# Kernel optimization log

Hardware: AMD Instinct MI355X
Metric: run time of the kernel (lower is better)

Reference implementation:

```python
import jax, jax.numpy as jnp
import numpy as np

T, B, E, H = 2048, 4, 768, 12
HD = E // H


def setup_inputs() -> dict:
    root = jax.random.key(0)
    ks = jax.random.split(root, 7)
    def xavier(k, shape):
        fan_in, fan_out = shape[1], shape[0]
        lim = (6.0 / (fan_in + fan_out)) ** 0.5
        return jax.random.uniform(k, shape, jnp.float32, -lim, lim)
    return {
        "query": jax.random.normal(ks[0], (T, B, E), jnp.float32),
        "key": jax.random.normal(ks[1], (T, B, E), jnp.float32),
        "value": jax.random.normal(ks[2], (T, B, E), jnp.float32),
        "in_proj_weight": xavier(ks[3], (3 * E, E)),
        "in_proj_bias": jnp.zeros((3 * E,), jnp.float32),
        "out_w": xavier(ks[4], (E, E)),
        "out_b": jnp.zeros((E,), jnp.float32),
    }


def reference(query, key, value, in_proj_weight, in_proj_bias, out_w, out_b):
    scaling = HD ** -0.5
    # separate Q/K/V projections from slices of the fused in_proj weight
    q = (query @ in_proj_weight[:E].T + in_proj_bias[:E]) * scaling
    k = key @ in_proj_weight[E:2 * E].T + in_proj_bias[E:2 * E]
    v = value @ in_proj_weight[2 * E:].T + in_proj_bias[2 * E:]
    tgt_len, bsz, _ = query.shape
    src_len = key.shape[0]
    # [T,B,E] -> [B,H,T,hd]
    qh = q.reshape(tgt_len, bsz, H, HD).transpose(1, 2, 0, 3)
    kh = k.reshape(src_len, bsz, H, HD).transpose(1, 2, 0, 3)
    vh = v.reshape(src_len, bsz, H, HD).transpose(1, 2, 0, 3)
    # full attention matrix [B,H,T,S] (faithful to the bmm-softmax-bmm impl)
    scores = jnp.einsum("bhqd,bhkd->bhqk", qh, kh)
    weights = jax.nn.softmax(scores, axis=-1)  # attn_dropout = 0.0 (eval)
    attn = jnp.einsum("bhqk,bhkd->bhqd", weights, vh)
    attn = attn.transpose(2, 0, 1, 3).reshape(tgt_len, bsz, E)
    out = attn @ out_w.T + out_b
    avg_weights = weights.sum(axis=1) / H  # [B,T,S]
    return out, avg_weights
```

## Files before the change

### kernel.cpp

```cpp
#include <hip/hip_runtime.h>

typedef unsigned short u16;
typedef unsigned long long u64;
typedef __attribute__((ext_vector_type(8))) short bf16x8;
typedef __attribute__((ext_vector_type(4))) float f32x4;
typedef __attribute__((ext_vector_type(16))) float f32x16;
typedef __attribute__((ext_vector_type(4))) _Float16 f16x4;
typedef __attribute__((ext_vector_type(2))) __fp16 h16x2;

#define TT 2048
#define BB 4
#define EE 768
#define HH 12
#define HD 64
#define NTOK 8192
#define KVB 32
#define NTILE (TT / KVB)

__device__ __forceinline__ u16 f2bf(float f) {
  unsigned int u = __builtin_bit_cast(unsigned int, f);
  u += 0x7fffu + ((u >> 16) & 1u);
  return (u16)(u >> 16);
}

__device__ __forceinline__ float bf2f(u16 b) {
  unsigned int u = (unsigned int)b << 16;
  return __builtin_bit_cast(float, u);
}

__device__ __forceinline__ unsigned int pack2(u16 a, u16 b) {
  return (unsigned int)a | ((unsigned int)b << 16);
}

__device__ __forceinline__ unsigned int pkh2(float a, float b) {
  h16x2 t = __builtin_amdgcn_cvt_pkrtz(a, b);
  return __builtin_bit_cast(unsigned int, t);
}

__global__ __launch_bounds__(256) void proj_qkv(
    const float* __restrict__ q_in, const float* __restrict__ k_in, const float* __restrict__ v_in,
    const float* __restrict__ ipw, const float* __restrict__ ipb,
    u16* __restrict__ qh, u16* __restrict__ kh, u16* __restrict__ vh)
{
  __shared__ u16 sA[128 * 40];
  __shared__ u16 sB[192 * 40];
  const int tid = threadIdx.x;
  const int w = tid >> 6, lane = tid & 63, l32 = lane & 31, hi = lane >> 5;
  const int wm = w & 1, wn = w >> 1;
  const int bn = blockIdx.x, bm = blockIdx.y, z = blockIdx.z;

  const float* A = (z == 0) ? q_in : (z == 1) ? k_in : v_in;
  const float* W = ipw + (size_t)z * EE * EE;
  const float* bias = ipb + z * EE;

  f32x16 acc[2][3] = {};

  for (int kt = 0; kt < EE / 32; ++kt) {
    __syncthreads();
#pragma unroll
    for (int i = 0; i < 4; ++i) {
      int c = i * 256 + tid;
      int row = c >> 3, cs = c & 7;
      const float4 v4 = *(const float4*)(A + (size_t)(bm * 128 + row) * EE + kt * 32 + cs * 4);
      u64 pk = (u64)pack2(f2bf(v4.x), f2bf(v4.y)) |
               ((u64)pack2(f2bf(v4.z), f2bf(v4.w)) << 32);
      *(u64*)&sA[row * 40 + cs * 4] = pk;
    }
#pragma unroll
    for (int i = 0; i < 6; ++i) {
      int c = i * 256 + tid;
      int row = c >> 3, cs = c & 7;
      const float4 v4 = *(const float4*)(W + (size_t)(bn * 192 + row) * EE + kt * 32 + cs * 4);
      u64 pk = (u64)pack2(f2bf(v4.x), f2bf(v4.y)) |
               ((u64)pack2(f2bf(v4.z), f2bf(v4.w)) << 32);
      *(u64*)&sB[row * 40 + cs * 4] = pk;
    }
    __syncthreads();
#pragma unroll
    for (int ks = 0; ks < 2; ++ks) {
      bf16x8 bfr[3];
#pragma unroll
      for (int tn = 0; tn < 3; ++tn)
        bfr[tn] = *(const bf16x8*)&sB[(wn * 96 + tn * 32 + l32) * 40 + ks * 16 + hi * 8];
#pragma unroll
      for (int tm = 0; tm < 2; ++tm) {
        bf16x8 afr = *(const bf16x8*)&sA[(wm * 64 + tm * 32 + l32) * 40 + ks * 16 + hi * 8];
#pragma unroll
        for (int tn = 0; tn < 3; ++tn)
          acc[tm][tn] = __builtin_amdgcn_mfma_f32_32x32x16_bf16(afr, bfr[tn], acc[tm][tn], 0, 0, 0);
      }
    }
  }

  const float scale = (z == 0) ? 0.125f : 1.0f;
  u16* dst = (z == 0) ? qh : (z == 1) ? kh : vh;
#pragma unroll
  for (int tn = 0; tn < 3; ++tn) {
    const int j = bn * 192 + wn * 96 + tn * 32 + l32;
    const int h = j >> 6, d = j & 63;
    const float bj = bias[j];
#pragma unroll
    for (int tm = 0; tm < 2; ++tm) {
#pragma unroll
      for (int r = 0; r < 16; ++r) {
        int m = bm * 128 + wm * 64 + tm * 32 + (r & 3) + 8 * (r >> 2) + 4 * hi;
        int t = m >> 2, bb = m & 3;
        float v = (acc[tm][tn][r] + bj) * scale;
        dst[((size_t)((bb * HH + h) * TT + t)) * HD + d] = f2bf(v);
      }
    }
  }
}

__global__ __launch_bounds__(256) void transpose_v(
    const u16* __restrict__ vh, _Float16* __restrict__ vhT)
{
  __shared__ u16 tile[64][72];
  const int tid = threadIdx.x;
  const int bh = blockIdx.y;
  const int t0 = blockIdx.x * 64;
  {
    int row = tid >> 2, seg = tid & 3;
    const u16* src = vh + (size_t)bh * TT * HD + (size_t)(t0 + row) * HD + seg * 16;
    uint4 a = *(const uint4*)(src);
    uint4 b = *(const uint4*)(src + 8);
    *(uint4*)&tile[row][seg * 16] = a;
    *(uint4*)&tile[row][seg * 16 + 8] = b;
  }
  __syncthreads();
  {
    int d = tid >> 2, ts = tid & 3;
    u16 tmp[16];
#pragma unroll
    for (int i = 0; i < 16; ++i) tmp[i] = tile[ts * 16 + i][d];
    unsigned int pk[8];
#pragma unroll
    for (int i = 0; i < 8; ++i)
      pk[i] = pkh2(bf2f(tmp[2 * i]), bf2f(tmp[2 * i + 1]));
    uint4 o0, o1;
    o0.x = pk[0]; o0.y = pk[1]; o0.z = pk[2]; o0.w = pk[3];
    o1.x = pk[4]; o1.y = pk[5]; o1.z = pk[6]; o1.w = pk[7];
    _Float16* dst = vhT + (size_t)bh * HD * TT + (size_t)d * TT + t0 + ts * 16;
    *(uint4*)dst = o0;
    *(uint4*)(dst + 8) = o1;
  }
}

__global__ __launch_bounds__(256, 3) void attn_flash(
    const u16* __restrict__ qh, const u16* __restrict__ kh, const _Float16* __restrict__ vhT,
    u16* __restrict__ ctx, float* __restrict__ stats_rl)
{
  __shared__ u16 sK[2][KVB * 64];
  __shared__ _Float16 sV[2][64 * 36];

  const int tid = threadIdx.x, w = tid >> 6, lane = tid & 63;
  const int l16 = lane & 15, quad = lane >> 4;
  const int orig = blockIdx.x;
  const int wg = (orig & 7) * 96 + (orig >> 3);
  const int qb = wg & 15;
  const int bhl = wg >> 4;
  const int b = bhl / HH, h = bhl - b * HH;
  const int q0 = qb * 128 + w * 32;
  const size_t bh = (size_t)bhl;
  const u16* qg = qh + (bh * TT + q0) * HD;
  const u16* kg = kh + bh * TT * HD;
  const _Float16* vg = vhT + bh * HD * TT;

  const int krow = tid >> 3, kch = tid & 7;
  const int kdst = krow * 64 + ((kch ^ (krow & 7)) * 8);
  const u16* kgp = kg + (size_t)krow * HD + kch * 8;
  const int vrow = tid >> 2, vch = tid & 3;
  const int vdst = vrow * 36 + vch * 8;
  const _Float16* vgp = vg + (size_t)vrow * TT + vch * 8;

  bf16x8 qf[2][2];
#pragma unroll
  for (int j = 0; j < 2; ++j)
#pragma unroll
    for (int p = 0; p < 2; ++p)
      qf[j][p] = *(const bf16x8*)(qg + (j * 16 + l16) * HD + p * 32 + quad * 8);

  f32x4 oacc[2][4] = {};
  float lsum[2] = {0.0f, 0.0f};

  {
    uint4 kv = *(const uint4*)kgp;
    uint4 vv = *(const uint4*)vgp;
    *(uint4*)&sK[0][kdst] = kv;
    *(u64*)&sV[0][vdst]     = ((const u64*)&vv)[0];
    *(u64*)&sV[0][vdst + 4] = ((const u64*)&vv)[1];
  }

  for (int st = 0; st < NTILE; ++st) {
    const int buf = st & 1;
    uint4 nk, nv;
    const bool more = (st + 1 < NTILE);
    if (more) {
      nk = *(const uint4*)(kgp + (size_t)(st + 1) * KVB * HD);
      nv = *(const uint4*)(vgp + (st + 1) * KVB);
    }
    __syncthreads();

    const u16* kb = &sK[buf][0];
    const _Float16* vb = &sV[buf][0];
#pragma unroll
    for (int ss = 0; ss < 2; ++ss) {
      const int krw = ss * 16 + l16;
      bf16x8 kf0 = *(const bf16x8*)&kb[krw * 64 + ((quad ^ (krw & 7)) * 8)];
      bf16x8 kf1 = *(const bf16x8*)&kb[krw * 64 + (((4 + quad) ^ (krw & 7)) * 8)];
      f16x4 vf[4];
#pragma unroll
      for (int m = 0; m < 4; ++m)
        vf[m] = *(const f16x4*)&vb[(m * 16 + l16) * 36 + ss * 16 + quad * 4];
#pragma unroll
      for (int j = 0; j < 2; ++j) {
        f32x4 z = {};
        f32x4 T = __builtin_amdgcn_mfma_f32_16x16x32_bf16(kf0, qf[j][0], z, 0, 0, 0);
        T = __builtin_amdgcn_mfma_f32_16x16x32_bf16(kf1, qf[j][1], T, 0, 0, 0);
        float p0 = __expf(T[0]), p1 = __expf(T[1]), p2 = __expf(T[2]), p3 = __expf(T[3]);
        lsum[j] += (p0 + p1) + (p2 + p3);
        uint2 uu;
        uu.x = pkh2(p0, p1);
        uu.y = pkh2(p2, p3);
        f16x4 pb = __builtin_bit_cast(f16x4, uu);
#pragma unroll
        for (int m = 0; m < 4; ++m)
          oacc[j][m] = __builtin_amdgcn_mfma_f32_16x16x16f16(vf[m], pb, oacc[j][m], 0, 0, 0);
      }
    }

    if (more) {
      const int nb = buf ^ 1;
      *(uint4*)&sK[nb][kdst] = nk;
      *(u64*)&sV[nb][vdst]     = ((const u64*)&nv)[0];
      *(u64*)&sV[nb][vdst + 4] = ((const u64*)&nv)[1];
    }
  }

#pragma unroll
  for (int j = 0; j < 2; ++j) {
    float s = lsum[j];
    s += __shfl_xor(s, 16);
    s += __shfl_xor(s, 32);
    float rl = 1.0f / s;
    const int q = q0 + j * 16 + l16;
    if (quad == 0) stats_rl[bh * TT + q] = rl;
    u16* crow = ctx + (size_t)(q * BB + b) * EE + h * HD;
#pragma unroll
    for (int m = 0; m < 4; ++m) {
      u64 pk =
          (u64)pack2(f2bf(oacc[j][m][0] * rl), f2bf(oacc[j][m][1] * rl)) |
          ((u64)pack2(f2bf(oacc[j][m][2] * rl), f2bf(oacc[j][m][3] * rl)) << 32);
      *(u64*)(crow + m * 16 + quad * 4) = pk;
    }
  }
}

__global__ __launch_bounds__(256) void attn_avg(
    const u16* __restrict__ qh, const u16* __restrict__ kh,
    const float* __restrict__ stats_rl, float* __restrict__ avg)
{
  const int tid = threadIdx.x, w = tid >> 6, lane = tid & 63;
  const int l16 = lane & 15, quad = lane >> 4;
  const int b = blockIdx.z;
  const int q0 = blockIdx.y * 128 + (w & 1) * 64;
  const int s0 = blockIdx.x * 128 + (w >> 1) * 64;

  f32x4 aacc[4][4] = {};

  for (int h = 0; h < HH; ++h) {
    const size_t bh = (size_t)(b * HH + h);
    const u16* qg = qh + (bh * TT + q0) * HD;
    const u16* kg = kh + (bh * TT + s0) * HD;

    bf16x8 qf[4][2], kf[4][2];
#pragma unroll
    for (int t = 0; t < 4; ++t)
#pragma unroll
      for (int ks = 0; ks < 2; ++ks) {
        qf[t][ks] = *(const bf16x8*)(qg + (t * 16 + l16) * HD + ks * 32 + quad * 8);
        kf[t][ks] = *(const bf16x8*)(kg + (t * 16 + l16) * HD + ks * 32 + quad * 8);
      }

    float4 lv[4];
#pragma unroll
    for (int tm = 0; tm < 4; ++tm)
      lv[tm] = *(const float4*)(stats_rl + bh * TT + q0 + tm * 16 + quad * 4);

#pragma unroll
    for (int nt = 0; nt < 4; ++nt) {
      f32x4 sacc[4] = {};
#pragma unroll
      for (int ks = 0; ks < 2; ++ks)
#pragma unroll
        for (int tm = 0; tm < 4; ++tm)
          sacc[tm] = __builtin_amdgcn_mfma_f32_16x16x32_bf16(qf[tm][ks], kf[nt][ks], sacc[tm], 0, 0, 0);
#pragma unroll
      for (int tm = 0; tm < 4; ++tm) {
        const float* rlp = (const float*)&lv[tm];
#pragma unroll
        for (int r = 0; r < 4; ++r)
          aacc[tm][nt][r] += __expf(sacc[tm][r]) * rlp[r];
      }
    }
  }

  const float ih = 1.0f / HH;
#pragma unroll
  for (int tm = 0; tm < 4; ++tm)
#pragma unroll
    for (int r = 0; r < 4; ++r) {
      int q = q0 + tm * 16 + quad * 4 + r;
#pragma unroll
      for (int nt = 0; nt < 4; ++nt)
        avg[((size_t)b * TT + q) * TT + s0 + nt * 16 + l16] = aacc[tm][nt][r] * ih;
    }
}

__global__ __launch_bounds__(256) void proj_out(
    const u16* __restrict__ ctx, const float* __restrict__ ow, const float* __restrict__ ob,
    float* __restrict__ out)
{
  __shared__ u16 sA[128 * 40];
  __shared__ u16 sB[64 * 40];
  const int tid = threadIdx.x;
  const int w = tid >> 6, lane = tid & 63, l32 = lane & 31, hi = lane >> 5;
  const int wm = w & 1, wn = w >> 1;
  const int bn = blockIdx.x, bm = blockIdx.y;

  f32x16 acc[2] = {};

  for (int kt = 0; kt < EE / 32; ++kt) {
    __syncthreads();
#pragma unroll
    for (int i = 0; i < 2; ++i) {
      int c = i * 256 + tid;
      int row = c >> 2, cs = c & 3;
      uint4 v4 = *(const uint4*)(ctx + (size_t)(bm * 128 + row) * EE + kt * 32 + cs * 8);
      *(uint4*)&sA[row * 40 + cs * 8] = v4;
    }
#pragma unroll
    for (int i = 0; i < 2; ++i) {
      int c = i * 256 + tid;
      int row = c >> 3, cs = c & 7;
      const float4 v4 = *(const float4*)(ow + (size_t)(bn * 64 + row) * EE + kt * 32 + cs * 4);
      u64 pk = (u64)pack2(f2bf(v4.x), f2bf(v4.y)) |
               ((u64)pack2(f2bf(v4.z), f2bf(v4.w)) << 32);
      *(u64*)&sB[row * 40 + cs * 4] = pk;
    }
    __syncthreads();
#pragma unroll
    for (int ks = 0; ks < 2; ++ks) {
      bf16x8 bfr = *(const bf16x8*)&sB[(wn * 32 + l32) * 40 + ks * 16 + hi * 8];
#pragma unroll
      for (int tm = 0; tm < 2; ++tm) {
        bf16x8 afr = *(const bf16x8*)&sA[(wm * 64 + tm * 32 + l32) * 40 + ks * 16 + hi * 8];
        acc[tm] = __builtin_amdgcn_mfma_f32_32x32x16_bf16(afr, bfr, acc[tm], 0, 0, 0);
      }
    }
  }

  const int j = bn * 64 + wn * 32 + l32;
  const float bj = ob[j];
#pragma unroll
  for (int tm = 0; tm < 2; ++tm) {
#pragma unroll
    for (int r = 0; r < 16; ++r) {
      int m = bm * 128 + wm * 64 + tm * 32 + (r & 3) + 8 * (r >> 2) + 4 * hi;
      out[(size_t)m * EE + j] = acc[tm][r] + bj;
    }
  }
}

extern "C" void kernel_launch(void* const* d_in, const int* in_sizes, int n_in,
                              void* d_out, int out_size, void* d_ws, size_t ws_size,
                              hipStream_t stream)
{
  const float* query = (const float*)d_in[0];
  const float* key   = (const float*)d_in[1];
  const float* value = (const float*)d_in[2];
  const float* ipw   = (const float*)d_in[3];
  const float* ipb   = (const float*)d_in[4];
  const float* ow    = (const float*)d_in[5];
  const float* ob    = (const float*)d_in[6];
  float* out = (float*)d_out;

  char* p = (char*)d_ws;
  const size_t QKV = (size_t)BB * HH * TT * HD * 2;
  u16* qh  = (u16*)p; p += QKV;
  u16* kh  = (u16*)p; p += QKV;
  u16* vh  = (u16*)p; p += QKV;
  _Float16* vhT = (_Float16*)p; p += QKV;
  u16* ctx = (u16*)p; p += (size_t)NTOK * EE * 2;
  float* stats = (float*)p;

  proj_qkv<<<dim3(4, 64, 3), 256, 0, stream>>>(query, key, value, ipw, ipb, qh, kh, vh);
  transpose_v<<<dim3(32, 48), 256, 0, stream>>>(vh, vhT);
  attn_flash<<<dim3(768, 1, 1), 256, 0, stream>>>(qh, kh, vhT, ctx, stats);
  attn_avg<<<dim3(16, 16, BB), 256, 0, stream>>>(qh, kh, stats, out + (size_t)NTOK * EE);
  proj_out<<<dim3(12, 64), 256, 0, stream>>>(ctx, ow, ob, out);
}
```

Baseline: 435.0 us.

## Double-buffer LDS with register prefetch in projection GEMMs and remap QKV blocks

```diff
diff --git a/kernel.cpp b/kernel.cpp
--- a/kernel.cpp
+++ b/kernel.cpp
@@ -32,48 +32,68 @@
   return (unsigned int)a | ((unsigned int)b << 16);
 }
 
+__device__ __forceinline__ unsigned int cvtpk2(float a, float b) {
+  unsigned int r;
+  asm("v_cvt_pk_bf16_f32 %0, %1, %2" : "=v"(r) : "v"(a), "v"(b));
+  return r;
+}
+
 __device__ __forceinline__ unsigned int pkh2(float a, float b) {
   h16x2 t = __builtin_amdgcn_cvt_pkrtz(a, b);
   return __builtin_bit_cast(unsigned int, t);
 }
 
-__global__ __launch_bounds__(256) void proj_qkv(
+__global__ __launch_bounds__(256, 3) void proj_qkv(
     const float* __restrict__ q_in, const float* __restrict__ k_in, const float* __restrict__ v_in,
     const float* __restrict__ ipw, const float* __restrict__ ipb,
     u16* __restrict__ qh, u16* __restrict__ kh, u16* __restrict__ vh)
 {
-  __shared__ u16 sA[128 * 40];
-  __shared__ u16 sB[192 * 40];
+  __shared__ u16 sA[2][128 * 40];
+  __shared__ u16 sB[2][192 * 40];
   const int tid = threadIdx.x;
   const int w = tid >> 6, lane = tid & 63, l32 = lane & 31, hi = lane >> 5;
   const int wm = w & 1, wn = w >> 1;
-  const int bn = blockIdx.x, bm = blockIdx.y, z = blockIdx.z;
+  const int orig = blockIdx.x;
+  const int wg = (orig & 7) * 96 + (orig >> 3);
+  const int z = wg >> 8;
+  const int rem = wg & 255;
+  const int bm = rem >> 2, bn = rem & 3;
 
   const float* A = (z == 0) ? q_in : (z == 1) ? k_in : v_in;
   const float* W = ipw + (size_t)z * EE * EE;
   const float* bias = ipb + z * EE;
 
+  const int srow = tid >> 3, scs = tid & 7;
+  const float* ag = A + (size_t)(bm * 128 + srow) * EE + scs * 4;
+  const float* wgp = W + (size_t)(bn * 192 + srow) * EE + scs * 4;
+
   f32x16 acc[2][3] = {};
+  float4 la[4], lw[6];
+
+#pragma unroll
+  for (int i = 0; i < 4; ++i) la[i] = *(const float4*)(ag + (size_t)i * 32 * EE);
+#pragma unroll
+  for (int i = 0; i < 6; ++i) lw[i] = *(const float4*)(wgp + (size_t)i * 32 * EE);
+#pragma unroll
+  for (int i = 0; i < 4; ++i) {
+    u64 pk = (u64)cvtpk2(la[i].x, la[i].y) | ((u64)cvtpk2(la[i].z, la[i].w) << 32);
+    *(u64*)&sA[0][(i * 32 + srow) * 40 + scs * 4] = pk;
+  }
+#pragma unroll
+  for (int i = 0; i < 6; ++i) {
+    u64 pk = (u64)cvtpk2(lw[i].x, lw[i].y) | ((u64)cvtpk2(lw[i].z, lw[i].w) << 32);
+    *(u64*)&sB[0][(i * 32 + srow) * 40 + scs * 4] = pk;
+  }
 
   for (int kt = 0; kt < EE / 32; ++kt) {
-    __syncthreads();
-#pragma unroll
-    for (int i = 0; i < 4; ++i) {
-      int c = i * 256 + tid;
-      int row = c >> 3, cs = c & 7;
-      const float4 v4 = *(const float4*)(A + (size_t)(bm * 128 + row) * EE + kt * 32 + cs * 4);
-      u64 pk = (u64)pack2(f2bf(v4.x), f2bf(v4.y)) |
-               ((u64)pack2(f2bf(v4.z), f2bf(v4.w)) << 32);
-      *(u64*)&sA[row * 40 + cs * 4] = pk;
-    }
-#pragma unroll
-    for (int i = 0; i < 6; ++i) {
-      int c = i * 256 + tid;
-      int row = c >> 3, cs = c & 7;
-      const float4 v4 = *(const float4*)(W + (size_t)(bn * 192 + row) * EE + kt * 32 + cs * 4);
-      u64 pk = (u64)pack2(f2bf(v4.x), f2bf(v4.y)) |
-               ((u64)pack2(f2bf(v4.z), f2bf(v4.w)) << 32);
-      *(u64*)&sB[row * 40 + cs * 4] = pk;
+    const int buf = kt & 1;
+    const bool more = (kt + 1) < EE / 32;
+    if (more) {
+      const int ko = (kt + 1) * 32;
+#pragma unroll
+      for (int i = 0; i < 4; ++i) la[i] = *(const float4*)(ag + (size_t)i * 32 * EE + ko);
+#pragma unroll
+      for (int i = 0; i < 6; ++i) lw[i] = *(const float4*)(wgp + (size_t)i * 32 * EE + ko);
     }
     __syncthreads();
 #pragma unroll
@@ -81,13 +101,26 @@
       bf16x8 bfr[3];
 #pragma unroll
       for (int tn = 0; tn < 3; ++tn)
-        bfr[tn] = *(const bf16x8*)&sB[(wn * 96 + tn * 32 + l32) * 40 + ks * 16 + hi * 8];
+        bfr[tn] = *(const bf16x8*)&sB[buf][(wn * 96 + tn * 32 + l32) * 40 + ks * 16 + hi * 8];
 #pragma unroll
       for (int tm = 0; tm < 2; ++tm) {
-        bf16x8 afr = *(const bf16x8*)&sA[(wm * 64 + tm * 32 + l32) * 40 + ks * 16 + hi * 8];
+        bf16x8 afr = *(const bf16x8*)&sA[buf][(wm * 64 + tm * 32 + l32) * 40 + ks * 16 + hi * 8];
 #pragma unroll
         for (int tn = 0; tn < 3; ++tn)
           acc[tm][tn] = __builtin_amdgcn_mfma_f32_32x32x16_bf16(afr, bfr[tn], acc[tm][tn], 0, 0, 0);
+      }
+    }
+    if (more) {
+      const int nb = buf ^ 1;
+#pragma unroll
+      for (int i = 0; i < 4; ++i) {
+        u64 pk = (u64)cvtpk2(la[i].x, la[i].y) | ((u64)cvtpk2(la[i].z, la[i].w) << 32);
+        *(u64*)&sA[nb][(i * 32 + srow) * 40 + scs * 4] = pk;
+      }
+#pragma unroll
+      for (int i = 0; i < 6; ++i) {
+        u64 pk = (u64)cvtpk2(lw[i].x, lw[i].y) | ((u64)cvtpk2(lw[i].z, lw[i].w) << 32);
+        *(u64*)&sB[nb][(i * 32 + srow) * 40 + scs * 4] = pk;
       }
     }
   }
@@ -317,45 +350,67 @@
     }
 }
 
-__global__ __launch_bounds__(256) void proj_out(
+__global__ __launch_bounds__(256, 3) void proj_out(
     const u16* __restrict__ ctx, const float* __restrict__ ow, const float* __restrict__ ob,
     float* __restrict__ out)
 {
-  __shared__ u16 sA[128 * 40];
-  __shared__ u16 sB[64 * 40];
+  __shared__ u16 sA[2][128 * 40];
+  __shared__ u16 sB[2][64 * 40];
   const int tid = threadIdx.x;
   const int w = tid >> 6, lane = tid & 63, l32 = lane & 31, hi = lane >> 5;
   const int wm = w & 1, wn = w >> 1;
   const int bn = blockIdx.x, bm = blockIdx.y;
 
+  const int arow = tid >> 2, acs = tid & 3;
+  const u16* ag = ctx + (size_t)(bm * 128 + arow) * EE + acs * 8;
+  const int brow = tid >> 3, bcs = tid & 7;
+  const float* wg2 = ow + (size_t)(bn * 64 + brow) * EE + bcs * 4;
+
   f32x16 acc[2] = {};
+  uint4 lca[2]; float4 lwb[2];
+
+#pragma unroll
+  for (int i = 0; i < 2; ++i) lca[i] = *(const uint4*)(ag + (size_t)i * 64 * EE);
+#pragma unroll
+  for (int i = 0; i < 2; ++i) lwb[i] = *(const float4*)(wg2 + (size_t)i * 32 * EE);
+#pragma unroll
+  for (int i = 0; i < 2; ++i)
+    *(uint4*)&sA[0][(i * 64 + arow) * 40 + acs * 8] = lca[i];
+#pragma unroll
+  for (int i = 0; i < 2; ++i) {
+    u64 pk = (u64)cvtpk2(lwb[i].x, lwb[i].y) | ((u64)cvtpk2(lwb[i].z, lwb[i].w) << 32);
+    *(u64*)&sB[0][(i * 32 + brow) * 40 + bcs * 4] = pk;
+  }
 
   for (int kt = 0; kt < EE / 32; ++kt) {
+    const int buf = kt & 1;
+    const bool more = (kt + 1) < EE / 32;
+    if (more) {
+      const int ko = (kt + 1) * 32;
+#pragma unroll
+      for (int i = 0; i < 2; ++i) lca[i] = *(const uint4*)(ag + (size_t)i * 64 * EE + ko);
+#pragma unroll
+      for (int i = 0; i < 2; ++i) lwb[i] = *(const float4*)(wg2 + (size_t)i * 32 * EE + ko);
+    }
     __syncthreads();
 #pragma unroll
-    for (int i = 0; i < 2; ++i) {
-      int c = i * 256 + tid;
-      int row = c >> 2, cs = c & 3;
-      uint4 v4 = *(const uint4*)(ctx + (size_t)(bm * 128 + row) * EE + kt * 32 + cs * 8);
-      *(uint4*)&sA[row * 40 + cs * 8] = v4;
-    }
-#pragma unroll
-    for (int i = 0; i < 2; ++i) {
-      int c = i * 256 + tid;
-      int row = c >> 3, cs = c & 7;
-      const float4 v4 = *(const float4*)(ow + (size_t)(bn * 64 + row) * EE + kt * 32 + cs * 4);
-      u64 pk = (u64)pack2(f2bf(v4.x), f2bf(v4.y)) |
-               ((u64)pack2(f2bf(v4.z), f2bf(v4.w)) << 32);
-      *(u64*)&sB[row * 40 + cs * 4] = pk;
-    }
-    __syncthreads();
-#pragma unroll
     for (int ks = 0; ks < 2; ++ks) {
-      bf16x8 bfr = *(const bf16x8*)&sB[(wn * 32 + l32) * 40 + ks * 16 + hi * 8];
+      bf16x8 bfr = *(const bf16x8*)&sB[buf][(wn * 32 + l32) * 40 + ks * 16 + hi * 8];
 #pragma unroll
       for (int tm = 0; tm < 2; ++tm) {
-        bf16x8 afr = *(const bf16x8*)&sA[(wm * 64 + tm * 32 + l32) * 40 + ks * 16 + hi * 8];
+        bf16x8 afr = *(const bf16x8*)&sA[buf][(wm * 64 + tm * 32 + l32) * 40 + ks * 16 + hi * 8];
         acc[tm] = __builtin_amdgcn_mfma_f32_32x32x16_bf16(afr, bfr, acc[tm], 0, 0, 0);
+      }
+    }
+    if (more) {
+      const int nb = buf ^ 1;
+#pragma unroll
+      for (int i = 0; i < 2; ++i)
+        *(uint4*)&sA[nb][(i * 64 + arow) * 40 + acs * 8] = lca[i];
+#pragma unroll
+      for (int i = 0; i < 2; ++i) {
+        u64 pk = (u64)cvtpk2(lwb[i].x, lwb[i].y) | ((u64)cvtpk2(lwb[i].z, lwb[i].w) << 32);
+        *(u64*)&sB[nb][(i * 32 + brow) * 40 + bcs * 4] = pk;
       }
     }
   }
@@ -394,7 +449,7 @@
   u16* ctx = (u16*)p; p += (size_t)NTOK * EE * 2;
   float* stats = (float*)p;
 
-  proj_qkv<<<dim3(4, 64, 3), 256, 0, stream>>>(query, key, value, ipw, ipb, qh, kh, vh);
+  proj_qkv<<<dim3(768, 1, 1), 256, 0, stream>>>(query, key, value, ipw, ipb, qh, kh, vh);
   transpose_v<<<dim3(32, 48), 256, 0, stream>>>(vh, vhT);
   attn_flash<<<dim3(768, 1, 1), 256, 0, stream>>>(qh, kh, vhT, ctx, stats);
   attn_avg<<<dim3(16, 16, BB), 256, 0, stream>>>(qh, kh, stats, out + (size_t)NTOK * EE);
```

Result: faster. 421.8 us (-3.0%).
